# Optimization experiments

Hardware: AMD Instinct MI355X
Metric: run time of the kernel (lower is better)

The kernel has to match this reference:

```python
import jax, jax.numpy as jnp
import numpy as np

N_HEAD = 16
TAU = 2.0          # gumbel-softmax temperature
CLAMP = 40.0       # safe_clamp bound for float32
NEG = -1e9         # mask value (stands in for strictly-causal exclusion)


def setup_inputs() -> dict:
    key = jax.random.key(0)
    k1, k2, k3 = jax.random.split(key, 3)
    B, T, E = 2, 2048, 1024
    hidden_states = jax.random.normal(k1, (B, T, E), jnp.float32)
    # nn.MultiheadAttention packed in-projection: rows [0:E]=Q, [E:2E]=K, [2E:3E]=V
    in_proj_weight = jax.random.normal(k2, (3 * E, E), jnp.float32) * 0.02
    in_proj_bias = jax.random.normal(k3, (3 * E,), jnp.float32) * 0.02
    return {
        "hidden_states": hidden_states,
        "in_proj_weight": in_proj_weight,
        "in_proj_bias": in_proj_bias,
    }


def reference(hidden_states, in_proj_weight, in_proj_bias):
    B, T, E = hidden_states.shape
    H = N_HEAD
    D = E // H
    # Only Q/K projections affect the output (attn_out / V / out_proj are discarded
    # by the original module, which uses only the attention weights).
    wq, wk = in_proj_weight[:E], in_proj_weight[E:2 * E]
    bq, bk = in_proj_bias[:E], in_proj_bias[E:2 * E]
    q = (hidden_states @ wq.T + bq).reshape(B, T, H, D)
    k = (hidden_states @ wk.T + bk).reshape(B, T, H, D)

    scale = 1.0 / jnp.sqrt(jnp.float32(D))
    scores = jnp.einsum('bqhd,bkhd->bhqk', q, k) * scale  # [B,H,T,T]

    idx = jnp.arange(T)
    valid = idx[None, :] < idx[:, None]                   # key strictly before query
    scores = jnp.where(valid[None, None], scores, NEG)
    probs = jax.nn.softmax(scores, axis=-1)               # per-head attn weights
    avg = probs.mean(axis=1)                              # average over heads [B,T,T]
    avg = jnp.clip(avg, -CLAMP, CLAMP)                    # safe_clamp (no-op for probs)

    # Gumbel-softmax reweighting (original re-seeds per step from data; here we use
    # a fixed key for deterministic, vectorized sampling).
    logits = jnp.where(valid[None], avg, NEG)
    u = jax.random.uniform(jax.random.key(42), (B, T, T), jnp.float32, 1e-6, 1.0 - 1e-6)
    gumbel = -jnp.log(-jnp.log(u))
    dw = jax.nn.softmax((logits + gumbel) / TAU, axis=-1)  # [B,T,T]

    out = jnp.einsum('btk,bke->bte', dw, hidden_states)    # weighted raw context
    # t == 0 has no context -> zeros
    return jnp.where((idx > 0)[None, :, None], out, 0.0)
```

## Files before the change

kernel.cpp:

```cpp
#include <hip/hip_runtime.h>
#include <math.h>

#define TT 2048
#define EE 1024
#define HH 16
#define DD 64
#define BB 2

typedef __bf16 bf16_t;
typedef __attribute__((ext_vector_type(8))) __bf16 bf16x8;
typedef __attribute__((ext_vector_type(4))) float f32x4;

__device__ __forceinline__ unsigned short f2b(float v) {
    return __builtin_bit_cast(unsigned short, (__bf16)v);
}

__device__ __forceinline__ void gll16(const void* g, void* l) {
    __builtin_amdgcn_global_load_lds(
        (const __attribute__((address_space(1))) void*)g,
        (__attribute__((address_space(3))) void*)l, 16, 0, 0);
}

__device__ __forceinline__ unsigned int rotl32(unsigned int x, int r) {
    return (x << r) | (x >> (32 - r));
}

__device__ __forceinline__ float gumbel_for(unsigned int f) {
    const unsigned int ks0 = 0u;
    const unsigned int ks1 = 42u;
    const unsigned int ks2 = 0x1BD11BDAu ^ ks0 ^ ks1;

    unsigned int v0 = 0u + ks0;
    unsigned int v1 = f  + ks1;

    v0 += v1; v1 = rotl32(v1, 13); v1 ^= v0;
    v0 += v1; v1 = rotl32(v1, 15); v1 ^= v0;
    v0 += v1; v1 = rotl32(v1, 26); v1 ^= v0;
    v0 += v1; v1 = rotl32(v1,  6); v1 ^= v0;
    v0 += ks1; v1 += ks2 + 1u;
    v0 += v1; v1 = rotl32(v1, 17); v1 ^= v0;
    v0 += v1; v1 = rotl32(v1, 29); v1 ^= v0;
    v0 += v1; v1 = rotl32(v1, 16); v1 ^= v0;
    v0 += v1; v1 = rotl32(v1, 24); v1 ^= v0;
    v0 += ks2; v1 += ks0 + 2u;
    v0 += v1; v1 = rotl32(v1, 13); v1 ^= v0;
    v0 += v1; v1 = rotl32(v1, 15); v1 ^= v0;
    v0 += v1; v1 = rotl32(v1, 26); v1 ^= v0;
    v0 += v1; v1 = rotl32(v1,  6); v1 ^= v0;
    v0 += ks0; v1 += ks1 + 3u;
    v0 += v1; v1 = rotl32(v1, 17); v1 ^= v0;
    v0 += v1; v1 = rotl32(v1, 29); v1 ^= v0;
    v0 += v1; v1 = rotl32(v1, 16); v1 ^= v0;
    v0 += v1; v1 = rotl32(v1, 24); v1 ^= v0;
    v0 += ks1; v1 += ks2 + 4u;
    v0 += v1; v1 = rotl32(v1, 13); v1 ^= v0;
    v0 += v1; v1 = rotl32(v1, 15); v1 ^= v0;
    v0 += v1; v1 = rotl32(v1, 26); v1 ^= v0;
    v0 += v1; v1 = rotl32(v1,  6); v1 ^= v0;
    v0 += ks2; v1 += ks0 + 5u;

    unsigned int bits = v0 ^ v1;
    unsigned int fb = (bits >> 9) | 0x3F800000u;
    float u01 = __uint_as_float(fb) - 1.0f;
    const float mn = 1e-6f;
    const float mx = 1.0f - 1e-6f;
    float u = fmaxf(mn, u01 * (mx - mn) + mn);
    return -__logf(-__logf(u));
}

__global__ __launch_bounds__(256) void convert_kernel(
    const float* __restrict__ hs, const float* __restrict__ W,
    bf16_t* __restrict__ hsbf, bf16_t* __restrict__ Wbf)
{
    const int n1 = BB * TT * EE / 4;
    const int n2 = 2 * EE * EE / 4;
    const int total = n1 + n2;
    for (int idx = blockIdx.x * 256 + threadIdx.x; idx < total;
         idx += gridDim.x * 256) {
        float4 v = (idx < n1) ? ((const float4*)hs)[idx]
                              : ((const float4*)W)[idx - n1];
        ushort4 o;
        o.x = f2b(v.x); o.y = f2b(v.y); o.z = f2b(v.z); o.w = f2b(v.w);
        if (idx < n1) ((ushort4*)hsbf)[idx] = o;
        else          ((ushort4*)Wbf)[idx - n1] = o;
    }
}

__global__ __launch_bounds__(256) void transpose_kernel(
    const float* __restrict__ hs, bf16_t* __restrict__ hsT)
{
    __shared__ float ts[64][65];
    const int e0 = blockIdx.x * 64;
    const int t0 = blockIdx.y * 64;
    const int b  = blockIdx.z;
    const int tid = threadIdx.x;
#pragma unroll
    for (int it = 0; it < 16; ++it) {
        const int idx = it * 256 + tid;
        const int tr = idx >> 6, te = idx & 63;
        ts[tr][te] = hs[((size_t)(b * TT + t0 + tr)) * EE + e0 + te];
    }
    __syncthreads();
#pragma unroll
    for (int it = 0; it < 16; ++it) {
        const int idx = it * 256 + tid;
        const int er = idx >> 6, tc = idx & 63;
        hsT[((size_t)(b * EE + e0 + er)) * TT + t0 + tc] = (__bf16)ts[tc][er];
    }
}

template <int K>
__device__ __forceinline__ void gemm_mainloop(
    const bf16_t* __restrict__ A, const bf16_t* __restrict__ Bm,
    int row0, int col0, int wave, int lane,
    bf16_t* Al0, bf16_t* Al1, bf16_t* Bl0, bf16_t* Bl1,
    f32x4 (&acc)[4][4])
{
    const int lrow = lane & 15;
    const int kgrp = lane >> 4;
    const int wr = wave >> 1, wc = wave & 1;
    const int lr4 = lane >> 2;
    const int sc  = (lane & 3) * 8;

    auto stage = [&](bf16_t* Ald, bf16_t* Bld, int k0) {
#pragma unroll
        for (int c = 0; c < 2; ++c) {
            const int srow = c * 64 + wave * 16;
            gll16(A  + (size_t)(row0 + srow + lr4) * K + k0 + sc, Ald + srow * 32);
            gll16(Bm + (size_t)(col0 + srow + lr4) * K + k0 + sc, Bld + srow * 32);
        }
    };
    auto compute = [&](const bf16_t* Ald, const bf16_t* Bld) {
        bf16x8 af[4], bfr[4];
#pragma unroll
        for (int m = 0; m < 4; ++m)
            af[m] = *(const bf16x8*)(Ald + (wr * 64 + m * 16 + lrow) * 32 + kgrp * 8);
#pragma unroll
        for (int n = 0; n < 4; ++n)
            bfr[n] = *(const bf16x8*)(Bld + (wc * 64 + n * 16 + lrow) * 32 + kgrp * 8);
#pragma unroll
        for (int m = 0; m < 4; ++m)
#pragma unroll
            for (int n = 0; n < 4; ++n)
                acc[m][n] = __builtin_amdgcn_mfma_f32_16x16x32_bf16(
                    af[m], bfr[n], acc[m][n], 0, 0, 0);
    };

    stage(Al0, Bl0, 0);
    __syncthreads();
#pragma unroll 1
    for (int t = 0; t < K / 32; t += 2) {
        stage(Al1, Bl1, (t + 1) * 32);
        compute(Al0, Bl0);
        __syncthreads();
        if (t + 2 < K / 32) stage(Al0, Bl0, (t + 2) * 32);
        compute(Al1, Bl1);
        __syncthreads();
    }
}

__global__ __launch_bounds__(256) void qk_gemm_kernel(
    const bf16_t* __restrict__ hsbf, const bf16_t* __restrict__ Wbf,
    const float* __restrict__ bias,
    bf16_t* __restrict__ Qbf, bf16_t* __restrict__ Kbf)
{
    __shared__ alignas(16) bf16_t Al0[128 * 32], Al1[128 * 32];
    __shared__ alignas(16) bf16_t Bl0[128 * 32], Bl1[128 * 32];

    const int wave = threadIdx.x >> 6;
    const int lane = threadIdx.x & 63;
    const int lrow = lane & 15;
    const int kgrp = lane >> 4;
    const int wr = wave >> 1, wc = wave & 1;
    const int row0 = blockIdx.y * 128;
    const int col0 = blockIdx.x * 128;

    f32x4 acc[4][4] = {};
    gemm_mainloop<EE>(hsbf, Wbf, row0, col0, wave, lane, Al0, Al1, Bl0, Bl1, acc);

#pragma unroll
    for (int n = 0; n < 4; ++n) {
        const int cc = col0 + wc * 64 + n * 16 + lrow;
        const float bv = bias[cc];
#pragma unroll
        for (int m = 0; m < 4; ++m) {
#pragma unroll
            for (int r = 0; r < 4; ++r) {
                const int rr = row0 + wr * 64 + m * 16 + 4 * kgrp + r;
                const float v = acc[m][n][r] + bv;
                const int b = rr >> 11, t = rr & (TT - 1);
                if (cc < EE) {
                    Qbf[(size_t)rr * EE + cc] = (__bf16)v;
                } else {
                    const int h = (cc - EE) >> 6, d = (cc - EE) & 63;
                    Kbf[(((size_t)(b * HH + h)) * TT + t) * DD + d] = (__bf16)v;
                }
            }
        }
    }
}

__global__ __launch_bounds__(256) void out_gemm_kernel(
    const bf16_t* __restrict__ dwbf, const bf16_t* __restrict__ hsT,
    const float* __restrict__ rowinv, float* __restrict__ out)
{
    __shared__ alignas(16) bf16_t Al0[128 * 32], Al1[128 * 32];
    __shared__ alignas(16) bf16_t Bl0[128 * 32], Bl1[128 * 32];

    const int wave = threadIdx.x >> 6;
    const int lane = threadIdx.x & 63;
    const int lrow = lane & 15;
    const int kgrp = lane >> 4;
    const int wr = wave >> 1, wc = wave & 1;
    const int b = blockIdx.z;
    const int row0 = blockIdx.y * 128;
    const int col0 = blockIdx.x * 128;

    const bf16_t* A  = dwbf + (size_t)b * TT * TT;
    const bf16_t* Bm = hsT  + (size_t)b * EE * TT;

    f32x4 acc[4][4] = {};
    gemm_mainloop<TT>(A, Bm, row0, col0, wave, lane, Al0, Al1, Bl0, Bl1, acc);

    float ri[4][4];
#pragma unroll
    for (int m = 0; m < 4; ++m)
#pragma unroll
        for (int r = 0; r < 4; ++r)
            ri[m][r] = rowinv[b * TT + row0 + wr * 64 + m * 16 + 4 * kgrp + r];

#pragma unroll
    for (int n = 0; n < 4; ++n) {
        const int cc = col0 + wc * 64 + n * 16 + lrow;
#pragma unroll
        for (int m = 0; m < 4; ++m) {
#pragma unroll
            for (int r = 0; r < 4; ++r) {
                const int rr = row0 + wr * 64 + m * 16 + 4 * kgrp + r;
                out[(size_t)(b * TT + rr) * EE + cc] = acc[m][n][r] * ri[m][r];
            }
        }
    }
}

__global__ __launch_bounds__(256) void rowsum_kernel(
    const bf16_t* __restrict__ Qbf, const bf16_t* __restrict__ Kbf,
    float* __restrict__ invl_g)
{
    __shared__ float rsp[4][64];
    const int tid = threadIdx.x;
    const int wave = tid >> 6;
    const int lane = tid & 63;
    const int lrow = lane & 15;
    const int kgrp = lane >> 4;
    const int h = blockIdx.y, b = blockIdx.z;
    const bf16_t* Kh = Kbf + (size_t)(b * HH + h) * TT * DD;

#pragma unroll 1
    for (int pick = 0; pick < 2; ++pick) {
        const int it = pick ? (31 - blockIdx.x) : blockIdx.x;
        const int i0 = it * 64;

        bf16x8 af[4][2];
        const bf16_t* qb = Qbf + (size_t)(b * TT + i0 + lrow) * EE + h * DD;
#pragma unroll
        for (int m = 0; m < 4; ++m) {
            af[m][0] = *(const bf16x8*)(qb + (size_t)(m * 16) * EE + kgrp * 8);
            af[m][1] = *(const bf16x8*)(qb + (size_t)(m * 16) * EE + 32 + kgrp * 8);
        }

        f32x4 rs[4] = {};
#pragma unroll 1
        for (int jt = wave; jt <= it; jt += 4) {
            const int j0 = jt * 64;
            const bf16_t* kb = Kh + (size_t)(j0 + lrow) * DD;
            bf16x8 bk[4][2];
#pragma unroll
            for (int n = 0; n < 4; ++n) {
                bk[n][0] = *(const bf16x8*)(kb + (size_t)(n * 16) * DD + kgrp * 8);
                bk[n][1] = *(const bf16x8*)(kb + (size_t)(n * 16) * DD + 32 + kgrp * 8);
            }
#pragma unroll
            for (int m = 0; m < 4; ++m) {
                f32x4 s[4];
#pragma unroll
                for (int n = 0; n < 4; ++n) {
                    s[n] = f32x4{0.f, 0.f, 0.f, 0.f};
                    s[n] = __builtin_amdgcn_mfma_f32_16x16x32_bf16(af[m][0], bk[n][0], s[n], 0, 0, 0);
                    s[n] = __builtin_amdgcn_mfma_f32_16x16x32_bf16(af[m][1], bk[n][1], s[n], 0, 0, 0);
                }
                if (jt == it) {
#pragma unroll
                    for (int n = 0; n < 4; ++n)
#pragma unroll
                        for (int r = 0; r < 4; ++r) {
                            const int jj = j0 + n * 16 + lrow;
                            const int ii = i0 + m * 16 + 4 * kgrp + r;
                            if (jj < ii) rs[m][r] += __expf(0.125f * s[n][r]);
                        }
                } else {
#pragma unroll
                    for (int n = 0; n < 4; ++n)
#pragma unroll
                        for (int r = 0; r < 4; ++r)
                            rs[m][r] += __expf(0.125f * s[n][r]);
                }
            }
        }
#pragma unroll
        for (int off = 1; off < 16; off <<= 1)
#pragma unroll
            for (int m = 0; m < 4; ++m)
#pragma unroll
                for (int r = 0; r < 4; ++r)
                    rs[m][r] += __shfl_xor(rs[m][r], off);
        if (lrow == 0) {
#pragma unroll
            for (int m = 0; m < 4; ++m)
#pragma unroll
                for (int r = 0; r < 4; ++r)
                    rsp[wave][m * 16 + 4 * kgrp + r] = rs[m][r];
        }
        __syncthreads();
        if (tid < 64) {
            const float tot = rsp[0][tid] + rsp[1][tid] + rsp[2][tid] + rsp[3][tid];
            invl_g[(size_t)(b * HH + h) * TT + i0 + tid] =
                (tot > 0.f) ? 1.0f / (tot * (float)HH) : 0.f;
        }
        __syncthreads();
    }
}

__global__ __launch_bounds__(256) void dw_tile_kernel(
    const bf16_t* __restrict__ Qbf, const bf16_t* __restrict__ Kbf,
    const float* __restrict__ invl_g, bf16_t* __restrict__ dwbf)
{
    __shared__ alignas(16) bf16_t kbuf[2][64 * 64];
    __shared__ alignas(16) bf16_t stile[64][72];

    const int wave = threadIdx.x >> 6;
    const int lane = threadIdx.x & 63;
    const int lrow = lane & 15;
    const int kgrp = lane >> 4;
    const int tid = threadIdx.x;
    const int b = blockIdx.y;

    const int tidx = (blockIdx.x & 7) * 66 + (blockIdx.x >> 3);

    int it = (int)((sqrtf(8.0f * tidx + 1.0f) - 1.0f) * 0.5f);
    while ((it + 1) * (it + 2) / 2 <= tidx) ++it;
    while (it * (it + 1) / 2 > tidx) --it;
    const int jt = tidx - it * (it + 1) / 2;
    const bool diag = (it == jt);
    const int i0 = it * 64, j0 = jt * 64;
    const int m = wave;
    const int rbase = i0 + m * 16;
    const int nlim = diag ? (m + 1) : 4;

    int prow[2], pchunk[2];
#pragma unroll
    for (int c = 0; c < 2; ++c) {
        const int p = wave * 2048 + c * 1024 + lane * 16;
        prow[c] = p >> 7;
        pchunk[c] = ((p >> 4) & 7) ^ (prow[c] & 7);
    }
    const bf16_t* Kb0 = Kbf + ((size_t)b * HH * TT + j0) * DD;

    auto stage = [&](int h, int buf) {
#pragma unroll
        for (int c = 0; c < 2; ++c) {
            gll16(Kb0 + (size_t)h * TT * DD + prow[c] * DD + pchunk[c] * 8,
                  (bf16_t*)kbuf[buf] + wave * 1024 + c * 512);
        }
    };

    const bf16_t* qbase = Qbf + (size_t)(b * TT + rbase + lrow) * EE;
    const float*  ribase = invl_g + (size_t)b * HH * TT + rbase + 4 * kgrp;
    const int swz0 = (kgrp ^ (lrow & 7)) * 8;
    const int swz1 = ((4 + kgrp) ^ (lrow & 7)) * 8;

    f32x4 avg[4] = {};

    stage(0, 0);

#pragma unroll 1
    for (int h = 0; h < HH; ++h) {
        const int cur = h & 1;
        const bf16_t* qb = qbase + h * DD;
        const bf16x8 a0 = *(const bf16x8*)(qb + kgrp * 8);
        const bf16x8 a1 = *(const bf16x8*)(qb + 32 + kgrp * 8);
        const f32x4 ric = *(const f32x4*)(ribase + (size_t)h * TT);
        if (h + 1 < HH) stage(h + 1, cur ^ 1);
        asm volatile("s_waitcnt vmcnt(2)" ::: "memory");
        __builtin_amdgcn_s_barrier();

        const bf16_t* kb = kbuf[cur];
        f32x4 s[4];
#pragma unroll
        for (int n = 0; n < 4; ++n) {
            if (n < nlim) {
                const int row = n * 16 + lrow;
                const bf16x8 b0 = *(const bf16x8*)(kb + row * 64 + swz0);
                const bf16x8 b1 = *(const bf16x8*)(kb + row * 64 + swz1);
                s[n] = f32x4{0.f, 0.f, 0.f, 0.f};
                s[n] = __builtin_amdgcn_mfma_f32_16x16x32_bf16(a0, b0, s[n], 0, 0, 0);
                s[n] = __builtin_amdgcn_mfma_f32_16x16x32_bf16(a1, b1, s[n], 0, 0, 0);
            }
        }
#pragma unroll
        for (int n = 0; n < 4; ++n) {
            if (n < nlim) {
#pragma unroll
                for (int r = 0; r < 4; ++r)
                    avg[n][r] += __expf(0.125f * s[n][r]) * ric[r];
            }
        }
        __builtin_amdgcn_s_barrier();
    }

#pragma unroll
    for (int n = 0; n < 4; ++n) {
        const int jj = j0 + n * 16 + lrow;
#pragma unroll
        for (int r = 0; r < 4; ++r) {
            const int rloc = m * 16 + 4 * kgrp + r;
            const int ii = i0 + rloc;
            float val = 0.f;
            if (n < nlim && jj < ii) {
                const float lg = fminf(fmaxf(avg[n][r], -40.0f), 40.0f);
                const float g = gumbel_for((unsigned)(b * TT + ii) * TT + (unsigned)jj);
                val = __expf((lg + g) * 0.5f);
            }
            stile[rloc][n * 16 + lrow] = (__bf16)val;
        }
    }
    __syncthreads();

#pragma unroll
    for (int p = 0; p < 2; ++p) {
        const int idx = p * 256 + tid;
        const int row = idx >> 3, cg = idx & 7;
        *(bf16x8*)(dwbf + (size_t)(b * TT + i0 + row) * TT + j0 + cg * 8) =
            *(const bf16x8*)(&stile[row][cg * 8]);
    }
}

__global__ __launch_bounds__(256) void rowinv_kernel(
    const bf16_t* __restrict__ dwbf, float* __restrict__ rowinv)
{
    __shared__ float red[256];
    const int blk = blockIdx.x;
    const int i = blk & (TT - 1);
    const int tid = threadIdx.x;
    const bf16_t* row = dwbf + (size_t)blk * TT;

    bf16x8 v = *(const bf16x8*)(row + tid * 8);
    float s = 0.f;
#pragma unroll
    for (int e = 0; e < 8; ++e) s += (float)v[e];
    red[tid] = s; __syncthreads();
    for (int st = 128; st > 0; st >>= 1) {
        if (tid < st) red[tid] += red[tid + st];
        __syncthreads();
    }
    if (tid == 0)
        rowinv[blk] = (i > 0 && red[0] > 0.f) ? 1.0f / red[0] : 0.f;
}

extern "C" void kernel_launch(void* const* d_in, const int* in_sizes, int n_in,
                              void* d_out, int out_size, void* d_ws, size_t ws_size,
                              hipStream_t stream) {
    const float* hs   = (const float*)d_in[0];
    const float* W    = (const float*)d_in[1];
    const float* bias = (const float*)d_in[2];
    float* out = (float*)d_out;

    char* ws = (char*)d_ws;
    bf16_t* dwbf   = (bf16_t*)ws;
    bf16_t* Qbf    = (bf16_t*)(ws + (size_t)16 * 1024 * 1024);
    bf16_t* Kbf    = (bf16_t*)(ws + (size_t)24 * 1024 * 1024);
    bf16_t* hsbf   = (bf16_t*)(ws + (size_t)32 * 1024 * 1024);
    bf16_t* Wbf    = (bf16_t*)(ws + (size_t)40 * 1024 * 1024);
    bf16_t* hsT    = (bf16_t*)(ws + (size_t)44 * 1024 * 1024);
    float*  invl_g = (float*) (ws + (size_t)52 * 1024 * 1024);
    float*  rowinv = (float*) (ws + (size_t)52 * 1024 * 1024 + 256 * 1024);

    hipMemsetAsync(dwbf, 0, (size_t)16 * 1024 * 1024, stream);
    convert_kernel<<<2048, 256, 0, stream>>>(hs, W, hsbf, Wbf);
    transpose_kernel<<<dim3(EE / 64, TT / 64, BB), 256, 0, stream>>>(hs, hsT);
    qk_gemm_kernel<<<dim3(2048 / 128, 4096 / 128), 256, 0, stream>>>(hsbf, Wbf, bias, Qbf, Kbf);
    rowsum_kernel<<<dim3(16, HH, BB), 256, 0, stream>>>(Qbf, Kbf, invl_g);
    dw_tile_kernel<<<dim3(528, BB), 256, 0, stream>>>(Qbf, Kbf, invl_g, dwbf);
    rowinv_kernel<<<BB * TT, 256, 0, stream>>>(dwbf, rowinv);
    out_gemm_kernel<<<dim3(EE / 128, TT / 128, BB), 256, 0, stream>>>(dwbf, hsT, rowinv, out);
}
```

Baseline: 159.4 us.

## Fuse hidden-state bf16 cast into transpose and process two heads per dw iteration

The bf16 conversion of hidden_states now happens inside the transpose kernel, which already reads hs, so hs is read once instead of twice and the convert kernel only handles W. The dw_tile kernel stages K tiles for two heads at a time, which halves the number of barrier and wait rounds in the head loop. It reuses the K buffer as the output staging tile to keep LDS use bounded. The costs are a larger LDS footprint per block, which may lower occupancy, and scalar bf16 stores in the transpose that may coalesce less well.

```diff
diff --git a/kernel.cpp b/kernel.cpp
--- a/kernel.cpp
+++ b/kernel.cpp
@@ -69,25 +69,21 @@
 }
 
 __global__ __launch_bounds__(256) void convert_kernel(
-    const float* __restrict__ hs, const float* __restrict__ W,
-    bf16_t* __restrict__ hsbf, bf16_t* __restrict__ Wbf)
-{
-    const int n1 = BB * TT * EE / 4;
-    const int n2 = 2 * EE * EE / 4;
-    const int total = n1 + n2;
+    const float* __restrict__ W, bf16_t* __restrict__ Wbf)
+{
+    const int total = 2 * EE * EE / 4;
     for (int idx = blockIdx.x * 256 + threadIdx.x; idx < total;
          idx += gridDim.x * 256) {
-        float4 v = (idx < n1) ? ((const float4*)hs)[idx]
-                              : ((const float4*)W)[idx - n1];
+        float4 v = ((const float4*)W)[idx];
         ushort4 o;
         o.x = f2b(v.x); o.y = f2b(v.y); o.z = f2b(v.z); o.w = f2b(v.w);
-        if (idx < n1) ((ushort4*)hsbf)[idx] = o;
-        else          ((ushort4*)Wbf)[idx - n1] = o;
+        ((ushort4*)Wbf)[idx] = o;
     }
 }
 
 __global__ __launch_bounds__(256) void transpose_kernel(
-    const float* __restrict__ hs, bf16_t* __restrict__ hsT)
+    const float* __restrict__ hs, bf16_t* __restrict__ hsbf,
+    bf16_t* __restrict__ hsT)
 {
     __shared__ float ts[64][65];
     const int e0 = blockIdx.x * 64;
@@ -98,7 +94,9 @@
     for (int it = 0; it < 16; ++it) {
         const int idx = it * 256 + tid;
         const int tr = idx >> 6, te = idx & 63;
-        ts[tr][te] = hs[((size_t)(b * TT + t0 + tr)) * EE + e0 + te];
+        const float v = hs[((size_t)(b * TT + t0 + tr)) * EE + e0 + te];
+        ts[tr][te] = v;
+        hsbf[((size_t)(b * TT + t0 + tr)) * EE + e0 + te] = (__bf16)v;
     }
     __syncthreads();
 #pragma unroll
@@ -335,8 +333,7 @@
     const bf16_t* __restrict__ Qbf, const bf16_t* __restrict__ Kbf,
     const float* __restrict__ invl_g, bf16_t* __restrict__ dwbf)
 {
-    __shared__ alignas(16) bf16_t kbuf[2][64 * 64];
-    __shared__ alignas(16) bf16_t stile[64][72];
+    __shared__ alignas(16) bf16_t kbuf[2][2][64 * 64];
 
     const int wave = threadIdx.x >> 6;
     const int lane = threadIdx.x & 63;
@@ -366,11 +363,14 @@
     }
     const bf16_t* Kb0 = Kbf + ((size_t)b * HH * TT + j0) * DD;
 
-    auto stage = [&](int h, int buf) {
-#pragma unroll
-        for (int c = 0; c < 2; ++c) {
-            gll16(Kb0 + (size_t)h * TT * DD + prow[c] * DD + pchunk[c] * 8,
-                  (bf16_t*)kbuf[buf] + wave * 1024 + c * 512);
+    auto stage = [&](int hp, int buf) {
+#pragma unroll
+        for (int hh = 0; hh < 2; ++hh) {
+#pragma unroll
+            for (int c = 0; c < 2; ++c) {
+                gll16(Kb0 + (size_t)(2 * hp + hh) * TT * DD + prow[c] * DD + pchunk[c] * 8,
+                      (bf16_t*)kbuf[buf][hh] + wave * 1024 + c * 512);
+            }
         }
     };
 
@@ -384,39 +384,50 @@
     stage(0, 0);
 
 #pragma unroll 1
-    for (int h = 0; h < HH; ++h) {
-        const int cur = h & 1;
-        const bf16_t* qb = qbase + h * DD;
-        const bf16x8 a0 = *(const bf16x8*)(qb + kgrp * 8);
-        const bf16x8 a1 = *(const bf16x8*)(qb + 32 + kgrp * 8);
-        const f32x4 ric = *(const f32x4*)(ribase + (size_t)h * TT);
-        if (h + 1 < HH) stage(h + 1, cur ^ 1);
-        asm volatile("s_waitcnt vmcnt(2)" ::: "memory");
+    for (int hp = 0; hp < HH / 2; ++hp) {
+        const int cur = hp & 1;
+        const bf16_t* qb0 = qbase + (2 * hp) * DD;
+        const bf16x8 a0h0 = *(const bf16x8*)(qb0 + kgrp * 8);
+        const bf16x8 a1h0 = *(const bf16x8*)(qb0 + 32 + kgrp * 8);
+        const bf16x8 a0h1 = *(const bf16x8*)(qb0 + DD + kgrp * 8);
+        const bf16x8 a1h1 = *(const bf16x8*)(qb0 + DD + 32 + kgrp * 8);
+        const f32x4 ri0 = *(const f32x4*)(ribase + (size_t)(2 * hp) * TT);
+        const f32x4 ri1 = *(const f32x4*)(ribase + (size_t)(2 * hp + 1) * TT);
+        if (hp + 1 < HH / 2) stage(hp + 1, cur ^ 1);
+        asm volatile("s_waitcnt vmcnt(4)" ::: "memory");
         __builtin_amdgcn_s_barrier();
 
-        const bf16_t* kb = kbuf[cur];
-        f32x4 s[4];
-#pragma unroll
-        for (int n = 0; n < 4; ++n) {
-            if (n < nlim) {
-                const int row = n * 16 + lrow;
-                const bf16x8 b0 = *(const bf16x8*)(kb + row * 64 + swz0);
-                const bf16x8 b1 = *(const bf16x8*)(kb + row * 64 + swz1);
-                s[n] = f32x4{0.f, 0.f, 0.f, 0.f};
-                s[n] = __builtin_amdgcn_mfma_f32_16x16x32_bf16(a0, b0, s[n], 0, 0, 0);
-                s[n] = __builtin_amdgcn_mfma_f32_16x16x32_bf16(a1, b1, s[n], 0, 0, 0);
-            }
-        }
-#pragma unroll
-        for (int n = 0; n < 4; ++n) {
-            if (n < nlim) {
-#pragma unroll
-                for (int r = 0; r < 4; ++r)
-                    avg[n][r] += __expf(0.125f * s[n][r]) * ric[r];
+#pragma unroll
+        for (int hh = 0; hh < 2; ++hh) {
+            const bf16_t* kb = kbuf[cur][hh];
+            const bf16x8 a0 = hh ? a0h1 : a0h0;
+            const bf16x8 a1 = hh ? a1h1 : a1h0;
+            const f32x4 ric = hh ? ri1 : ri0;
+            f32x4 s[4];
+#pragma unroll
+            for (int n = 0; n < 4; ++n) {
+                if (n < nlim) {
+                    const int row = n * 16 + lrow;
+                    const bf16x8 b0 = *(const bf16x8*)(kb + row * 64 + swz0);
+                    const bf16x8 b1 = *(const bf16x8*)(kb + row * 64 + swz1);
+                    s[n] = f32x4{0.f, 0.f, 0.f, 0.f};
+                    s[n] = __builtin_amdgcn_mfma_f32_16x16x32_bf16(a0, b0, s[n], 0, 0, 0);
+                    s[n] = __builtin_amdgcn_mfma_f32_16x16x32_bf16(a1, b1, s[n], 0, 0, 0);
+                }
+            }
+#pragma unroll
+            for (int n = 0; n < 4; ++n) {
+                if (n < nlim) {
+#pragma unroll
+                    for (int r = 0; r < 4; ++r)
+                        avg[n][r] += __expf(0.125f * s[n][r]) * ric[r];
+                }
             }
         }
         __builtin_amdgcn_s_barrier();
     }
+
+    bf16_t (*stile)[72] = (bf16_t(*)[72])&kbuf[0][0][0];
 
 #pragma unroll
     for (int n = 0; n < 4; ++n) {
@@ -486,8 +497,8 @@
     float*  rowinv = (float*) (ws + (size_t)52 * 1024 * 1024 + 256 * 1024);
 
     hipMemsetAsync(dwbf, 0, (size_t)16 * 1024 * 1024, stream);
-    convert_kernel<<<2048, 256, 0, stream>>>(hs, W, hsbf, Wbf);
-    transpose_kernel<<<dim3(EE / 64, TT / 64, BB), 256, 0, stream>>>(hs, hsT);
+    convert_kernel<<<1024, 256, 0, stream>>>(W, Wbf);
+    transpose_kernel<<<dim3(EE / 64, TT / 64, BB), 256, 0, stream>>>(hs, hsbf, hsT);
     qk_gemm_kernel<<<dim3(2048 / 128, 4096 / 128), 256, 0, stream>>>(hsbf, Wbf, bias, Qbf, Kbf);
     rowsum_kernel<<<dim3(16, HH, BB), 256, 0, stream>>>(Qbf, Kbf, invl_g);
     dw_tile_kernel<<<dim3(528, BB), 256, 0, stream>>>(Qbf, Kbf, invl_g, dwbf);
```

After: 159.5 us. No clear change (+0.1%).
